# Performance work log

Measured on AMD Instinct MI355X. Metric: run time of the kernel, lower is better.

## Reference

```python
import jax, jax.numpy as jnp
import numpy as np

N_NODES = 100000
N_HEDGES = 25000
NNZ = 1600000
IN_CH = 128
HEADS_OUT = 128  # heads * out_channels = 8 * 16


def setup_inputs() -> dict:
    key = jax.random.key(0)
    k1, k2, k3, k4, k5, k6 = jax.random.split(key, 6)
    X = jax.random.normal(k1, (N_NODES, IN_CH), dtype=jnp.float32)
    Wlin = jax.random.normal(k2, (IN_CH, HEADS_OUT), dtype=jnp.float32) * (1.0 / np.sqrt(IN_CH))
    degE = jax.random.uniform(k3, (N_HEDGES, 1), dtype=jnp.float32)
    degV = jax.random.uniform(k4, (N_NODES, 1), dtype=jnp.float32)
    W = jnp.ones((N_HEDGES, 1), dtype=jnp.float32)
    g1_src = jax.random.randint(k5, (NNZ,), 0, N_NODES, dtype=jnp.int32)
    g1_dst = jax.random.randint(k6, (NNZ,), 0, N_HEDGES, dtype=jnp.int32)
    return {"X": X, "Wlin": Wlin, "degE": degE, "degV": degV, "W": W,
            "g1_src": g1_src, "g1_dst": g1_dst}


def reference(X, Wlin, degE, degV, W, g1_src, g1_dst):
    # Linear projection (no bias): [N, in_ch] @ [in_ch, heads*out] -> [N, HO]
    Xp = X @ Wlin
    # Stage 1: copy_u_sum over g1 (node -> hyperedge): out[e] = sum_{v in e} Xp[v]
    Xe = jax.ops.segment_sum(Xp[g1_src], g1_dst, num_segments=N_HEDGES)
    # Elementwise hyperedge scaling: degE then W (W is ones buffer in original)
    Xe = Xe * degE * W
    # Stage 2: copy_u_sum over g2 = g1^T (hyperedge -> node)
    Xv = jax.ops.segment_sum(Xe[g1_dst], g1_src, num_segments=N_NODES)
    # Node degree scaling
    Xv = Xv * degV
    return Xv
```

## Files before the change

kernel.cpp:

```cpp
#include <hip/hip_runtime.h>
#include <hip/hip_bf16.h>


#define CAPE 128
#define CAPV 64
#define LDK  136
#define RW   6250

typedef __attribute__((ext_vector_type(8))) short bf16x8;
typedef __attribute__((ext_vector_type(4))) float f32x4;
typedef __attribute__((ext_vector_type(8))) float f32x8;

__device__ __forceinline__ unsigned short f32_to_bf16(float f) {
    unsigned int u = __float_as_uint(f);
    u += 0x7FFFu + ((u >> 16) & 1u);
    return (unsigned short)(u >> 16);
}
__device__ __forceinline__ float bf16_to_f32(unsigned short h) {
    return __uint_as_float(((unsigned int)h) << 16);
}


__device__ __forceinline__ void scan_body(unsigned char* __restrict__ h8, int n,
                                          int b, int nch, int* __restrict__ cnt) {
    int run = 0;
    for (int c0 = 0; c0 < nch; c0 += 16) {
        unsigned char v[16];
#pragma unroll
        for (int j = 0; j < 16; ++j)
            v[j] = h8[(long)(c0 + j) * n + b];
        unsigned char w[16];
#pragma unroll
        for (int j = 0; j < 16; ++j) {
            w[j] = (unsigned char)run;
            run += v[j];
        }
#pragma unroll
        for (int j = 0; j < 16; ++j)
            h8[(long)(c0 + j) * n + b] = w[j];
    }
    cnt[b] = run;
}

__device__ __forceinline__ void hist_body(unsigned int* __restrict__ s32,
                                          const int* __restrict__ key, int nnz,
                                          unsigned int* __restrict__ hist,
                                          int n4, int ch, int c, int w0, int w1,
                                          int tid) {
    const int nw = w1 - w0;
    for (int i = tid; i < nw; i += 256) s32[i] = 0;
    __syncthreads();
    int e0 = c * ch, e1 = e0 + ch; if (e1 > nnz) e1 = nnz;
    for (int e = e0 + tid; e < e1; e += 256) {
        int k = key[e];
        int w = k >> 2;
        if (w >= w0 && w < w1)
            atomicAdd(&s32[w - w0], 1u << ((k & 3) * 8));
    }
    __syncthreads();
    for (int i = tid; i < nw; i += 256)
        hist[(long)c * n4 + w0 + i] = s32[i];
}

__device__ __forceinline__ void scatV_body(unsigned int* __restrict__ c32,
                                           const int* __restrict__ src,
                                           const int* __restrict__ dst, int nnz,
                                           const unsigned char* __restrict__ histV8,
                                           unsigned short* __restrict__ adjV,
                                           int nV4, int chv, int c, int r, int tid) {
    const int w0 = r * RW;
    int w1 = w0 + RW; if (w1 > nV4) w1 = nV4;
    const int nw = w1 - w0;
    const unsigned int* brow = (const unsigned int*)histV8 + (long)c * nV4 + w0;
    for (int i = tid; i < nw; i += 256) c32[i] = brow[i];
    __syncthreads();
    int e0 = c * chv, e1 = e0 + chv; if (e1 > nnz) e1 = nnz;
    for (int e = e0 + tid; e < e1; e += 256) {
        int k = src[e];
        int w = k >> 2;
        if (w < w0 || w >= w1) continue;
        int sh = (k & 3) * 8;
        unsigned int old = atomicAdd(&c32[w - w0], 1u << sh);
        int slot = (old >> sh) & 0xFF;
        if (slot < CAPV) adjV[(long)k * CAPV + slot] = (unsigned short)dst[e];
    }
}

__device__ __forceinline__ void gatherE_body(int id, int tid,
                                             const unsigned short* __restrict__ Xp,
                                             const int* __restrict__ cntE,
                                             const int* __restrict__ adjE,
                                             const float* __restrict__ degE,
                                             const float* __restrict__ Wbuf,
                                             unsigned short* __restrict__ Xe,
                                             int nE) {
    int t = id * 256 + tid;
    int e = t >> 4;
    if (e >= nE) return;
    int c = (t & 15) << 3;
    int len = cntE[e];
    if (len > CAPE) len = CAPE;
    const int* adj = adjE + (long)e * CAPE;
    float acc[8];
#pragma unroll
    for (int q = 0; q < 8; ++q) acc[q] = 0.f;

    int i = 0;
    for (; i + 16 <= len; i += 16) {
        int4 a0 = *(const int4*)(adj + i);
        int4 a1 = *(const int4*)(adj + i + 4);
        int4 a2 = *(const int4*)(adj + i + 8);
        int4 a3 = *(const int4*)(adj + i + 12);
        int v[16] = {a0.x, a0.y, a0.z, a0.w, a1.x, a1.y, a1.z, a1.w,
                     a2.x, a2.y, a2.z, a2.w, a3.x, a3.y, a3.z, a3.w};
        bf16x8 h[16];
#pragma unroll
        for (int j = 0; j < 16; ++j)
            h[j] = *(const bf16x8*)(Xp + (long)v[j] * 128 + c);
#pragma unroll
        for (int j = 0; j < 16; ++j)
#pragma unroll
            for (int q = 0; q < 8; ++q)
                acc[q] += bf16_to_f32((unsigned short)h[j][q]);
    }
    for (; i + 8 <= len; i += 8) {
        int4 a0 = *(const int4*)(adj + i);
        int4 a1 = *(const int4*)(adj + i + 4);
        int v[8] = {a0.x, a0.y, a0.z, a0.w, a1.x, a1.y, a1.z, a1.w};
        bf16x8 h[8];
#pragma unroll
        for (int j = 0; j < 8; ++j)
            h[j] = *(const bf16x8*)(Xp + (long)v[j] * 128 + c);
#pragma unroll
        for (int j = 0; j < 8; ++j)
#pragma unroll
            for (int q = 0; q < 8; ++q)
                acc[q] += bf16_to_f32((unsigned short)h[j][q]);
    }
    for (; i + 4 <= len; i += 4) {
        int4 a0 = *(const int4*)(adj + i);
        int v[4] = {a0.x, a0.y, a0.z, a0.w};
        bf16x8 h[4];
#pragma unroll
        for (int j = 0; j < 4; ++j)
            h[j] = *(const bf16x8*)(Xp + (long)v[j] * 128 + c);
#pragma unroll
        for (int j = 0; j < 4; ++j)
#pragma unroll
            for (int q = 0; q < 8; ++q)
                acc[q] += bf16_to_f32((unsigned short)h[j][q]);
    }
    for (; i < len; ++i) {
        int v = adj[i];
        bf16x8 h = *(const bf16x8*)(Xp + (long)v * 128 + c);
#pragma unroll
        for (int q = 0; q < 8; ++q)
            acc[q] += bf16_to_f32((unsigned short)h[q]);
    }

    float sc = degE[e] * Wbuf[e];
    bf16x8 o;
#pragma unroll
    for (int q = 0; q < 8; ++q) o[q] = (short)f32_to_bf16(acc[q] * sc);
    *(bf16x8*)(Xe + (long)e * 128 + c) = o;
}

__device__ __forceinline__ void gatherV_body(int id, int tid,
                                             const unsigned short* __restrict__ Xe,
                                             const int* __restrict__ cntV,
                                             const unsigned short* __restrict__ adjV,
                                             const float* __restrict__ degV,
                                             float* __restrict__ out,
                                             int vLo, int vHi) {
    int t = id * 256 + tid;
    int v = vLo + (t >> 4);
    if (v >= vHi) return;
    int c = (t & 15) << 3;
    int len = cntV[v];
    if (len > CAPV) len = CAPV;
    const unsigned short* adj = adjV + (long)v * CAPV;
    float acc[8];
#pragma unroll
    for (int q = 0; q < 8; ++q) acc[q] = 0.f;

    int i = 0;
    for (; i + 16 <= len; i += 16) {
        ushort4 a0 = *(const ushort4*)(adj + i);
        ushort4 a1 = *(const ushort4*)(adj + i + 4);
        ushort4 a2 = *(const ushort4*)(adj + i + 8);
        ushort4 a3 = *(const ushort4*)(adj + i + 12);
        int e[16] = {a0.x, a0.y, a0.z, a0.w, a1.x, a1.y, a1.z, a1.w,
                     a2.x, a2.y, a2.z, a2.w, a3.x, a3.y, a3.z, a3.w};
        bf16x8 h[16];
#pragma unroll
        for (int j = 0; j < 16; ++j)
            h[j] = *(const bf16x8*)(Xe + (long)e[j] * 128 + c);
#pragma unroll
        for (int j = 0; j < 16; ++j)
#pragma unroll
            for (int q = 0; q < 8; ++q)
                acc[q] += bf16_to_f32((unsigned short)h[j][q]);
    }
    for (; i + 8 <= len; i += 8) {
        ushort4 a0 = *(const ushort4*)(adj + i);
        ushort4 a1 = *(const ushort4*)(adj + i + 4);
        int e[8] = {a0.x, a0.y, a0.z, a0.w, a1.x, a1.y, a1.z, a1.w};
        bf16x8 h[8];
#pragma unroll
        for (int j = 0; j < 8; ++j)
            h[j] = *(const bf16x8*)(Xe + (long)e[j] * 128 + c);
#pragma unroll
        for (int j = 0; j < 8; ++j)
#pragma unroll
            for (int q = 0; q < 8; ++q)
                acc[q] += bf16_to_f32((unsigned short)h[j][q]);
    }
    for (; i + 4 <= len; i += 4) {
        ushort4 a0 = *(const ushort4*)(adj + i);
        int e[4] = {a0.x, a0.y, a0.z, a0.w};
        bf16x8 h[4];
#pragma unroll
        for (int j = 0; j < 4; ++j)
            h[j] = *(const bf16x8*)(Xe + (long)e[j] * 128 + c);
#pragma unroll
        for (int j = 0; j < 4; ++j)
#pragma unroll
            for (int q = 0; q < 8; ++q)
                acc[q] += bf16_to_f32((unsigned short)h[j][q]);
    }
    for (; i < len; ++i) {
        int e = adj[i];
        bf16x8 h = *(const bf16x8*)(Xe + (long)e * 128 + c);
#pragma unroll
        for (int q = 0; q < 8; ++q)
            acc[q] += bf16_to_f32((unsigned short)h[q]);
    }

    float sc = degV[v];
    f32x8 o;
#pragma unroll
    for (int q = 0; q < 8; ++q) o[q] = acc[q] * sc;
    *(f32x8*)(out + (long)v * 128 + c) = o;
}


__global__ __launch_bounds__(256) void k_init(const float* __restrict__ Wl,
                                              unsigned short* __restrict__ Wt) {
    int idx = blockIdx.x * 256 + threadIdx.x;
    if (idx < 128 * 128) {
        int n = idx >> 7, k = idx & 127;
        Wt[idx] = f32_to_bf16(Wl[k * 128 + n]);
    }
}

__global__ __launch_bounds__(256) void k_gemm_histE(
    const float* __restrict__ X, const unsigned short* __restrict__ Wt,
    unsigned short* __restrict__ Xp, int nrows, int nGemm,
    const int* __restrict__ keyE, int nnz,
    unsigned int* __restrict__ histE32, int nE4, int che, int nchE)
{
    __shared__ union {
        struct { unsigned short Xs[64 * LDK]; unsigned short Wt[128 * LDK]; } g;
        unsigned int s32[RW];
    } sm;

    int bid = blockIdx.x;
    const int tid = threadIdx.x;

    if (bid < nGemm) {
        const int row0 = bid * 64;
        for (int base = tid * 4; base < 64 * 128; base += 1024) {
            int r = base >> 7, c = base & 127;
            float4 v = make_float4(0.f, 0.f, 0.f, 0.f);
            if (row0 + r < nrows) v = *(const float4*)(X + (long)(row0 + r) * 128 + c);
            ushort4 h;
            h.x = f32_to_bf16(v.x); h.y = f32_to_bf16(v.y);
            h.z = f32_to_bf16(v.z); h.w = f32_to_bf16(v.w);
            *(ushort4*)(sm.g.Xs + r * LDK + c) = h;
        }
        for (int base = tid * 4; base < 128 * 128; base += 1024) {
            int n = base >> 7, k = base & 127;
            ushort4 h = *(const ushort4*)(Wt + base);
            *(ushort4*)(sm.g.Wt + n * LDK + k) = h;
        }
        __syncthreads();

        const int w    = tid >> 6;
        const int lane = tid & 63;
        const int m    = lane & 15;
        const int quad = lane >> 4;

        f32x4 acc[8];
#pragma unroll
        for (int ct = 0; ct < 8; ++ct) acc[ct] = (f32x4){0.f, 0.f, 0.f, 0.f};

#pragma unroll
        for (int kk = 0; kk < 4; ++kk) {
            bf16x8 a = *(const bf16x8*)(sm.g.Xs + (w * 16 + m) * LDK + kk * 32 + quad * 8);
#pragma unroll
            for (int ct = 0; ct < 8; ++ct) {
                bf16x8 b = *(const bf16x8*)(sm.g.Wt + (ct * 16 + m) * LDK + kk * 32 + quad * 8);
                acc[ct] = __builtin_amdgcn_mfma_f32_16x16x32_bf16(a, b, acc[ct], 0, 0, 0);
            }
        }
#pragma unroll
        for (int ct = 0; ct < 8; ++ct) {
#pragma unroll
            for (int r = 0; r < 4; ++r) {
                int row = row0 + w * 16 + quad * 4 + r;
                if (row < nrows)
                    Xp[(long)row * 128 + ct * 16 + m] = f32_to_bf16(acc[ct][r]);
            }
        }
        return;
    }

    int c = bid - nGemm;
    if (c < nchE)
        hist_body(sm.s32, keyE, nnz, histE32, nE4, che, c, 0, nE4, tid);
}

__global__ __launch_bounds__(256) void k_scanE_histV(
    unsigned char* __restrict__ histE8, int* __restrict__ cntE,
    int nE, int nchE, int nScanE,
    const int* __restrict__ keyV, int nnz,
    unsigned int* __restrict__ histV32, int nV4, int chv, int nchV)
{
    __shared__ unsigned int s32[RW];
    int bid = blockIdx.x;
    const int tid = threadIdx.x;
    if (bid < nScanE) {
        int t = bid * 256 + tid;
        if (t < nE) scan_body(histE8, nE, t, nchE, cntE);
        return;
    }
    bid -= nScanE;
    const int c = bid % nchV, r = bid / nchV;
    const int w0 = r * RW;
    int w1 = w0 + RW; if (w1 > nV4) w1 = nV4;
    hist_body(s32, keyV, nnz, histV32, nV4, chv, c, w0, w1, tid);
}

__global__ __launch_bounds__(256) void k_scatE_scanV(
    const int* __restrict__ src, const int* __restrict__ dst, int nnz,
    const unsigned char* __restrict__ histE8, int* __restrict__ adjE,
    int nE4, int che, int nchE,
    unsigned char* __restrict__ histV8, int* __restrict__ cntV, int nV, int nchV)
{
    __shared__ unsigned int c32[RW];
    int bid = blockIdx.x;
    const int tid = threadIdx.x;
    if (bid < nchE) {
        const int c = bid;
        const unsigned int* brow = (const unsigned int*)histE8 + (long)c * nE4;
        for (int i = tid; i < nE4; i += 256) c32[i] = brow[i];
        __syncthreads();
        int e0 = c * che, e1 = e0 + che; if (e1 > nnz) e1 = nnz;
        for (int e = e0 + tid; e < e1; e += 256) {
            int k = dst[e];
            int sh = (k & 3) * 8;
            unsigned int old = atomicAdd(&c32[k >> 2], 1u << sh);
            int slot = (old >> sh) & 0xFF;
            if (slot < CAPE) adjE[(long)k * CAPE + slot] = src[e];
        }
        return;
    }
    int t = (bid - nchE) * 256 + tid;
    if (t < nV) scan_body(histV8, nV, t, nchV, cntV);
}

__global__ __launch_bounds__(256) void k_gathE_scatV(
    const unsigned short* __restrict__ Xp, const int* __restrict__ cntE,
    const int* __restrict__ adjE, const float* __restrict__ degE,
    const float* __restrict__ Wbuf, unsigned short* __restrict__ Xe,
    int nE, int nGathE,
    const int* __restrict__ src, const int* __restrict__ dst, int nnz,
    const unsigned char* __restrict__ histV8, unsigned short* __restrict__ adjV,
    int nV4, int chv, int nchV)
{
    __shared__ unsigned int c32[RW];
    int bid = blockIdx.x;
    const int tid = threadIdx.x;
    if (bid < nGathE) {
        gatherE_body(bid, tid, Xp, cntE, adjE, degE, Wbuf, Xe, nE);
        return;
    }
    bid -= nGathE;
    const int c = bid % nchV, r = bid / nchV;
    scatV_body(c32, src, dst, nnz, histV8, adjV, nV4, chv, c, r, tid);
}

__global__ __launch_bounds__(256) void k_gatherV(const unsigned short* __restrict__ Xe,
                                                 const int* __restrict__ cntV,
                                                 const unsigned short* __restrict__ adjV,
                                                 const float* __restrict__ degV,
                                                 float* __restrict__ out,
                                                 int vLo, int vHi) {
    gatherV_body(blockIdx.x, threadIdx.x, Xe, cntV, adjV, degV, out, vLo, vHi);
}

__global__ __launch_bounds__(256) void zero_f4(float4* __restrict__ p, int n4) {
    int i = blockIdx.x * 256 + threadIdx.x;
    if (i < n4) p[i] = make_float4(0.f, 0.f, 0.f, 0.f);
}

__global__ __launch_bounds__(256) void gemm_xw_f32(const float* __restrict__ X,
                                                   const float* __restrict__ Wl,
                                                   float* __restrict__ Xp,
                                                   int nrows) {
    __shared__ float Xs[32 * 128];
    const int tid = threadIdx.x;
    const int row0 = blockIdx.x * 32;
    for (int i = tid * 4; i < 32 * 128; i += 256 * 4) {
        int r = row0 + (i >> 7);
        float4 v = make_float4(0.f, 0.f, 0.f, 0.f);
        if (r < nrows) v = *(const float4*)(X + (long)row0 * 128 + i);
        *(float4*)(Xs + i) = v;
    }
    __syncthreads();
    const int col = tid & 127;
    const int rg  = (tid >> 7) * 16;
    float acc[16];
#pragma unroll
    for (int r = 0; r < 16; ++r) acc[r] = 0.f;
    for (int k = 0; k < 128; k += 4) {
        const float w0 = Wl[(k + 0) * 128 + col];
        const float w1 = Wl[(k + 1) * 128 + col];
        const float w2 = Wl[(k + 2) * 128 + col];
        const float w3 = Wl[(k + 3) * 128 + col];
#pragma unroll
        for (int r = 0; r < 16; ++r) {
            float4 x = *(const float4*)(Xs + (rg + r) * 128 + k);
            acc[r] = fmaf(x.w, w3, fmaf(x.z, w2, fmaf(x.y, w1, fmaf(x.x, w0, acc[r]))));
        }
    }
#pragma unroll
    for (int r = 0; r < 16; ++r) {
        int row = row0 + rg + r;
        if (row < nrows) Xp[(long)row * 128 + col] = acc[r];
    }
}

__global__ __launch_bounds__(256) void scatter_to_hedges(const float* __restrict__ Xp,
                                                         const int* __restrict__ src,
                                                         const int* __restrict__ dst,
                                                         float* __restrict__ Xe,
                                                         int nnz) {
    int t = blockIdx.x * 256 + threadIdx.x;
    int e = t >> 5;
    if (e >= nnz) return;
    int c = (t & 31) << 2;
    int s = src[e], d = dst[e];
    float4 v = *(const float4*)(Xp + (long)s * 128 + c);
    float* o = Xe + (long)d * 128 + c;
    atomicAdd(o + 0, v.x); atomicAdd(o + 1, v.y);
    atomicAdd(o + 2, v.z); atomicAdd(o + 3, v.w);
}

__global__ __launch_bounds__(256) void scatter_to_nodes(const float* __restrict__ Xe,
                                                        const int* __restrict__ src,
                                                        const int* __restrict__ dst,
                                                        const float* __restrict__ degE,
                                                        const float* __restrict__ Wbuf,
                                                        const float* __restrict__ degV,
                                                        float* __restrict__ out,
                                                        int nnz) {
    int t = blockIdx.x * 256 + threadIdx.x;
    int e = t >> 5;
    if (e >= nnz) return;
    int c = (t & 31) << 2;
    int s = src[e], d = dst[e];
    float sc = degE[d] * Wbuf[d] * degV[s];
    float4 v = *(const float4*)(Xe + (long)d * 128 + c);
    float* o = out + (long)s * 128 + c;
    atomicAdd(o + 0, v.x * sc); atomicAdd(o + 1, v.y * sc);
    atomicAdd(o + 2, v.z * sc); atomicAdd(o + 3, v.w * sc);
}

extern "C" void kernel_launch(void* const* d_in, const int* in_sizes, int n_in,
                              void* d_out, int out_size, void* d_ws, size_t ws_size,
                              hipStream_t stream) {
    const float* X    = (const float*)d_in[0];
    const float* Wlin = (const float*)d_in[1];
    const float* degE = (const float*)d_in[2];
    const float* degV = (const float*)d_in[3];
    const float* Wbuf = (const float*)d_in[4];
    const int* g1_src = (const int*)d_in[5];
    const int* g1_dst = (const int*)d_in[6];

    const int nE  = in_sizes[2];
    const int nV  = in_sizes[3];
    const int nnz = in_sizes[5];

    float* out = (float*)d_out;
    char* ws = (char*)d_ws;

    auto layout_size = [&](int cE, int cV) -> size_t {
        size_t o = 0;
        o += (size_t)nE * CAPE * 4;
        o += (size_t)nV * CAPV * 2;
        o += (size_t)nE * 4 + (size_t)nV * 4;
        size_t he = (size_t)cE * nE;
        size_t xe = (size_t)nE * 128 * 2;
        o += (he > xe) ? he : xe;
        o += (size_t)cV * nV;
        o += 128 * 128 * 2;
        o += 4096;
        return o;
    };

    int nchE = 256, nchV = 256;
    if (layout_size(nchE, nchV) > ws_size) { nchE = 256; nchV = 128; }
    if (layout_size(nchE, nchV) > ws_size) { nchE = 128; nchV = 128; }
    if (layout_size(nchE, nchV) > ws_size) { nchE = 64;  nchV = 64;  }

    const int nE4 = nE >> 2, nV4 = nV >> 2;
    const bool eligible = ((nE & 3) == 0) && ((nV & 3) == 0) && (nE4 <= RW) &&
                          layout_size(nchE, nchV) <= ws_size;

    if (eligible) {
        size_t boff = 0;
        auto alloc = [&](size_t bytes) -> char* {
            char* p = ws + boff;
            boff += (bytes + 255) & ~(size_t)255;
            return p;
        };
        int* adjE            = (int*)alloc((size_t)nE * CAPE * 4);
        unsigned short* adjV = (unsigned short*)alloc((size_t)nV * CAPV * 2);
        int* cntE            = (int*)alloc((size_t)nE * 4);
        int* cntV            = (int*)alloc((size_t)nV * 4);
        size_t he = (size_t)nchE * nE;
        size_t xe = (size_t)nE * 128 * 2;
        char* region1         = alloc((he > xe) ? he : xe);
        unsigned char* histE8 = (unsigned char*)region1;
        unsigned short* Xe    = (unsigned short*)region1;
        unsigned char* histV8 = (unsigned char*)alloc((size_t)nchV * nV);
        unsigned short* Wt    = (unsigned short*)alloc((size_t)128 * 128 * 2);

        unsigned short* Xp_bf = (unsigned short*)d_out;

        const int nrV = (nV4 + RW - 1) / RW;
        const int che = (nnz + nchE - 1) / nchE;
        const int chv = (nnz + nchV - 1) / nchV;

        k_init<<<64, 256, 0, stream>>>(Wlin, Wt);

        int nGemm = (nV + 63) / 64;
        k_gemm_histE<<<nGemm + nchE, 256, 0, stream>>>(
            X, Wt, Xp_bf, nV, nGemm,
            g1_dst, nnz, (unsigned int*)histE8, nE4, che, nchE);

        int nScanE = (nE + 255) / 256;
        k_scanE_histV<<<nScanE + nchV * nrV, 256, 0, stream>>>(
            histE8, cntE, nE, nchE, nScanE,
            g1_src, nnz, (unsigned int*)histV8, nV4, chv, nchV);

        int nScanV = (nV + 255) / 256;
        k_scatE_scanV<<<nchE + nScanV, 256, 0, stream>>>(
            g1_src, g1_dst, nnz, histE8, adjE, nE4, che, nchE,
            histV8, cntV, nV, nchV);

        int nGathE = (nE * 16 + 255) / 256;
        k_gathE_scatV<<<nGathE + nchV * nrV, 256, 0, stream>>>(
            Xp_bf, cntE, adjE, degE, Wbuf, Xe, nE, nGathE,
            g1_src, g1_dst, nnz, histV8, adjV, nV4, chv, nchV);

        int nGathV = (nV * 16 + 255) / 256;
        k_gatherV<<<nGathV, 256, 0, stream>>>(Xe, cntV, adjV, degV, out, 0, nV);
    } else {
        float* XeF = (float*)d_ws;
        float* Xp  = out;
        int n4 = nE * 128 / 4;
        zero_f4<<<(n4 + 255) / 256, 256, 0, stream>>>((float4*)XeF, n4);
        gemm_xw_f32<<<(nV + 31) / 32, 256, 0, stream>>>(X, Wlin, Xp, nV);
        long th = (long)nnz * 32;
        scatter_to_hedges<<<(int)((th + 255) / 256), 256, 0, stream>>>(Xp, g1_src, g1_dst,
                                                                       XeF, nnz);
        int m4 = out_size / 4;
        zero_f4<<<(m4 + 255) / 256, 256, 0, stream>>>((float4*)out, m4);
        scatter_to_nodes<<<(int)((th + 255) / 256), 256, 0, stream>>>(XeF, g1_src, g1_dst,
                                                                      degE, Wbuf, degV,
                                                                      out, nnz);
    }
}
```

Before: 326.2 us.

## Store projected features in column-sliced layout and gather hyperedges per slice

After: 394.7 us. +21.0%, slower.

```diff
diff --git a/kernel.cpp b/kernel.cpp
--- a/kernel.cpp
+++ b/kernel.cpp
@@ -10,6 +10,8 @@
 typedef __attribute__((ext_vector_type(8))) short bf16x8;
 typedef __attribute__((ext_vector_type(4))) float f32x4;
 typedef __attribute__((ext_vector_type(8))) float f32x8;
+typedef __attribute__((ext_vector_type(4))) int i32x4;
+typedef __attribute__((ext_vector_type(4))) unsigned short u16x4;
 
 __device__ __forceinline__ unsigned short f32_to_bf16(float f) {
     unsigned int u = __float_as_uint(f);
@@ -82,22 +84,25 @@
         int sh = (k & 3) * 8;
         unsigned int old = atomicAdd(&c32[w - w0], 1u << sh);
         int slot = (old >> sh) & 0xFF;
-        if (slot < CAPV) adjV[(long)k * CAPV + slot] = (unsigned short)dst[e];
-    }
-}
-
-__device__ __forceinline__ void gatherE_body(int id, int tid,
-                                             const unsigned short* __restrict__ Xp,
-                                             const int* __restrict__ cntE,
-                                             const int* __restrict__ adjE,
-                                             const float* __restrict__ degE,
-                                             const float* __restrict__ Wbuf,
-                                             unsigned short* __restrict__ Xe,
-                                             int nE) {
-    int t = id * 256 + tid;
-    int e = t >> 4;
+        if (slot < CAPV)
+            __builtin_nontemporal_store((unsigned short)dst[e],
+                                        adjV + (long)k * CAPV + slot);
+    }
+}
+
+__device__ __forceinline__ void gatherE_sliced(int bid, int tid,
+                                               const unsigned short* __restrict__ Xp,
+                                               const int* __restrict__ cntE,
+                                               const int* __restrict__ adjE,
+                                               const float* __restrict__ degE,
+                                               const float* __restrict__ Wbuf,
+                                               unsigned short* __restrict__ Xe,
+                                               int nE, long sstride) {
+    const int slice = bid & 7;
+    int e = ((bid >> 3) << 7) + (tid >> 1);
     if (e >= nE) return;
-    int c = (t & 15) << 3;
+    const int c = (tid & 1) << 3;
+    const unsigned short* Xs = Xp + (long)slice * sstride;
     int len = cntE[e];
     if (len > CAPE) len = CAPE;
     const int* adj = adjE + (long)e * CAPE;
@@ -107,16 +112,16 @@
 
     int i = 0;
     for (; i + 16 <= len; i += 16) {
-        int4 a0 = *(const int4*)(adj + i);
-        int4 a1 = *(const int4*)(adj + i + 4);
-        int4 a2 = *(const int4*)(adj + i + 8);
-        int4 a3 = *(const int4*)(adj + i + 12);
+        i32x4 a0 = __builtin_nontemporal_load((const i32x4*)(adj + i));
+        i32x4 a1 = __builtin_nontemporal_load((const i32x4*)(adj + i + 4));
+        i32x4 a2 = __builtin_nontemporal_load((const i32x4*)(adj + i + 8));
+        i32x4 a3 = __builtin_nontemporal_load((const i32x4*)(adj + i + 12));
         int v[16] = {a0.x, a0.y, a0.z, a0.w, a1.x, a1.y, a1.z, a1.w,
                      a2.x, a2.y, a2.z, a2.w, a3.x, a3.y, a3.z, a3.w};
         bf16x8 h[16];
 #pragma unroll
         for (int j = 0; j < 16; ++j)
-            h[j] = *(const bf16x8*)(Xp + (long)v[j] * 128 + c);
+            h[j] = *(const bf16x8*)(Xs + (long)v[j] * 16 + c);
 #pragma unroll
         for (int j = 0; j < 16; ++j)
 #pragma unroll
@@ -124,13 +129,13 @@
                 acc[q] += bf16_to_f32((unsigned short)h[j][q]);
     }
     for (; i + 8 <= len; i += 8) {
-        int4 a0 = *(const int4*)(adj + i);
-        int4 a1 = *(const int4*)(adj + i + 4);
+        i32x4 a0 = __builtin_nontemporal_load((const i32x4*)(adj + i));
+        i32x4 a1 = __builtin_nontemporal_load((const i32x4*)(adj + i + 4));
         int v[8] = {a0.x, a0.y, a0.z, a0.w, a1.x, a1.y, a1.z, a1.w};
         bf16x8 h[8];
 #pragma unroll
         for (int j = 0; j < 8; ++j)
-            h[j] = *(const bf16x8*)(Xp + (long)v[j] * 128 + c);
+            h[j] = *(const bf16x8*)(Xs + (long)v[j] * 16 + c);
 #pragma unroll
         for (int j = 0; j < 8; ++j)
 #pragma unroll
@@ -138,12 +143,12 @@
                 acc[q] += bf16_to_f32((unsigned short)h[j][q]);
     }
     for (; i + 4 <= len; i += 4) {
-        int4 a0 = *(const int4*)(adj + i);
+        i32x4 a0 = __builtin_nontemporal_load((const i32x4*)(adj + i));
         int v[4] = {a0.x, a0.y, a0.z, a0.w};
         bf16x8 h[4];
 #pragma unroll
         for (int j = 0; j < 4; ++j)
-            h[j] = *(const bf16x8*)(Xp + (long)v[j] * 128 + c);
+            h[j] = *(const bf16x8*)(Xs + (long)v[j] * 16 + c);
 #pragma unroll
         for (int j = 0; j < 4; ++j)
 #pragma unroll
@@ -152,7 +157,7 @@
     }
     for (; i < len; ++i) {
         int v = adj[i];
-        bf16x8 h = *(const bf16x8*)(Xp + (long)v * 128 + c);
+        bf16x8 h = *(const bf16x8*)(Xs + (long)v * 16 + c);
 #pragma unroll
         for (int q = 0; q < 8; ++q)
             acc[q] += bf16_to_f32((unsigned short)h[q]);
@@ -162,7 +167,7 @@
     bf16x8 o;
 #pragma unroll
     for (int q = 0; q < 8; ++q) o[q] = (short)f32_to_bf16(acc[q] * sc);
-    *(bf16x8*)(Xe + (long)e * 128 + c) = o;
+    __builtin_nontemporal_store(o, (bf16x8*)(Xe + (long)e * 128 + slice * 16 + c));
 }
 
 __device__ __forceinline__ void gatherV_body(int id, int tid,
@@ -185,10 +190,10 @@
 
     int i = 0;
     for (; i + 16 <= len; i += 16) {
-        ushort4 a0 = *(const ushort4*)(adj + i);
-        ushort4 a1 = *(const ushort4*)(adj + i + 4);
-        ushort4 a2 = *(const ushort4*)(adj + i + 8);
-        ushort4 a3 = *(const ushort4*)(adj + i + 12);
+        u16x4 a0 = *(const u16x4*)(adj + i);
+        u16x4 a1 = *(const u16x4*)(adj + i + 4);
+        u16x4 a2 = *(const u16x4*)(adj + i + 8);
+        u16x4 a3 = *(const u16x4*)(adj + i + 12);
         int e[16] = {a0.x, a0.y, a0.z, a0.w, a1.x, a1.y, a1.z, a1.w,
                      a2.x, a2.y, a2.z, a2.w, a3.x, a3.y, a3.z, a3.w};
         bf16x8 h[16];
@@ -202,8 +207,8 @@
                 acc[q] += bf16_to_f32((unsigned short)h[j][q]);
     }
     for (; i + 8 <= len; i += 8) {
-        ushort4 a0 = *(const ushort4*)(adj + i);
-        ushort4 a1 = *(const ushort4*)(adj + i + 4);
+        u16x4 a0 = *(const u16x4*)(adj + i);
+        u16x4 a1 = *(const u16x4*)(adj + i + 4);
         int e[8] = {a0.x, a0.y, a0.z, a0.w, a1.x, a1.y, a1.z, a1.w};
         bf16x8 h[8];
 #pragma unroll
@@ -216,7 +221,7 @@
                 acc[q] += bf16_to_f32((unsigned short)h[j][q]);
     }
     for (; i + 4 <= len; i += 4) {
-        ushort4 a0 = *(const ushort4*)(adj + i);
+        u16x4 a0 = *(const u16x4*)(adj + i);
         int e[4] = {a0.x, a0.y, a0.z, a0.w};
         bf16x8 h[4];
 #pragma unroll
@@ -240,7 +245,7 @@
     f32x8 o;
 #pragma unroll
     for (int q = 0; q < 8; ++q) o[q] = acc[q] * sc;
-    *(f32x8*)(out + (long)v * 128 + c) = o;
+    __builtin_nontemporal_store(o, (f32x8*)(out + (long)v * 128 + c));
 }
 
 
@@ -309,7 +314,8 @@
             for (int r = 0; r < 4; ++r) {
                 int row = row0 + w * 16 + quad * 4 + r;
                 if (row < nrows)
-                    Xp[(long)row * 128 + ct * 16 + m] = f32_to_bf16(acc[ct][r]);
+                    Xp[(long)ct * nrows * 16 + (long)row * 16 + m] =
+                        f32_to_bf16(acc[ct][r]);
             }
         }
         return;
@@ -373,7 +379,7 @@
     const unsigned short* __restrict__ Xp, const int* __restrict__ cntE,
     const int* __restrict__ adjE, const float* __restrict__ degE,
     const float* __restrict__ Wbuf, unsigned short* __restrict__ Xe,
-    int nE, int nGathE,
+    int nE, int nGathE, long sstride,
     const int* __restrict__ src, const int* __restrict__ dst, int nnz,
     const unsigned char* __restrict__ histV8, unsigned short* __restrict__ adjV,
     int nV4, int chv, int nchV)
@@ -382,7 +388,7 @@
     int bid = blockIdx.x;
     const int tid = threadIdx.x;
     if (bid < nGathE) {
-        gatherE_body(bid, tid, Xp, cntE, adjE, degE, Wbuf, Xe, nE);
+        gatherE_sliced(bid, tid, Xp, cntE, adjE, degE, Wbuf, Xe, nE, sstride);
         return;
     }
     bid -= nGathE;
@@ -542,6 +548,7 @@
         const int nrV = (nV4 + RW - 1) / RW;
         const int che = (nnz + nchE - 1) / nchE;
         const int chv = (nnz + nchV - 1) / nchV;
+        const long sstride = (long)nV * 16;
 
         k_init<<<64, 256, 0, stream>>>(Wlin, Wt);
 
@@ -560,9 +567,9 @@
             g1_src, g1_dst, nnz, histE8, adjE, nE4, che, nchE,
             histV8, cntV, nV, nchV);
 
-        int nGathE = (nE * 16 + 255) / 256;
+        int nGathE = 8 * ((nE + 127) / 128);
         k_gathE_scatV<<<nGathE + nchV * nrV, 256, 0, stream>>>(
-            Xp_bf, cntE, adjE, degE, Wbuf, Xe, nE, nGathE,
+            Xp_bf, cntE, adjE, degE, Wbuf, Xe, nE, nGathE, sstride,
             g1_src, g1_dst, nnz, histV8, adjV, nV4, chv, nchV);
 
         int nGathV = (nV * 16 + 255) / 256;
```

## Split gathers into column halves and overlap second-half hedge gather with node gather

Applied to the files above, without the earlier changes.

New measurement: 327.2 us. About the same (+0.3%).

```diff
diff --git a/kernel.cpp b/kernel.cpp
--- a/kernel.cpp
+++ b/kernel.cpp
@@ -86,7 +86,7 @@
     }
 }
 
-__device__ __forceinline__ void gatherE_body(int id, int tid,
+__device__ __forceinline__ void gatherE_half(int id, int tid, int colBase,
                                              const unsigned short* __restrict__ Xp,
                                              const int* __restrict__ cntE,
                                              const int* __restrict__ adjE,
@@ -95,9 +95,9 @@
                                              unsigned short* __restrict__ Xe,
                                              int nE) {
     int t = id * 256 + tid;
-    int e = t >> 4;
+    int e = t >> 3;
     if (e >= nE) return;
-    int c = (t & 15) << 3;
+    int c = ((t & 7) << 3) + colBase;
     int len = cntE[e];
     if (len > CAPE) len = CAPE;
     const int* adj = adjE + (long)e * CAPE;
@@ -165,17 +165,17 @@
     *(bf16x8*)(Xe + (long)e * 128 + c) = o;
 }
 
-__device__ __forceinline__ void gatherV_body(int id, int tid,
+__device__ __forceinline__ void gatherV_half(int id, int tid, int colBase,
                                              const unsigned short* __restrict__ Xe,
                                              const int* __restrict__ cntV,
                                              const unsigned short* __restrict__ adjV,
                                              const float* __restrict__ degV,
                                              float* __restrict__ out,
-                                             int vLo, int vHi) {
+                                             int nV) {
     int t = id * 256 + tid;
-    int v = vLo + (t >> 4);
-    if (v >= vHi) return;
-    int c = (t & 15) << 3;
+    int v = t >> 3;
+    if (v >= nV) return;
+    int c = ((t & 7) << 3) + colBase;
     int len = cntV[v];
     if (len > CAPV) len = CAPV;
     const unsigned short* adj = adjV + (long)v * CAPV;
@@ -382,12 +382,38 @@
     int bid = blockIdx.x;
     const int tid = threadIdx.x;
     if (bid < nGathE) {
-        gatherE_body(bid, tid, Xp, cntE, adjE, degE, Wbuf, Xe, nE);
+        gatherE_half(bid, tid, 0, Xp, cntE, adjE, degE, Wbuf, Xe, nE);
         return;
     }
     bid -= nGathE;
     const int c = bid % nchV, r = bid / nchV;
     scatV_body(c32, src, dst, nnz, histV8, adjV, nV4, chv, c, r, tid);
+}
+
+__global__ __launch_bounds__(256) void k_gathE_gathV(
+    const unsigned short* __restrict__ Xp, const int* __restrict__ cntE,
+    const int* __restrict__ adjE, const float* __restrict__ degE,
+    const float* __restrict__ Wbuf, unsigned short* __restrict__ Xe,
+    int nE, int nGathE,
+    const int* __restrict__ cntV, const unsigned short* __restrict__ adjV,
+    const float* __restrict__ degV, float* __restrict__ out, int nV)
+{
+    int bid = blockIdx.x;
+    const int tid = threadIdx.x;
+    if (bid < nGathE) {
+        gatherE_half(bid, tid, 64, Xp, cntE, adjE, degE, Wbuf, Xe, nE);
+        return;
+    }
+    gatherV_half(bid - nGathE, tid, 0, Xe, cntV, adjV, degV, out, nV);
+}
+
+__global__ __launch_bounds__(256) void k_gathE_only(
+    const unsigned short* __restrict__ Xp, const int* __restrict__ cntE,
+    const int* __restrict__ adjE, const float* __restrict__ degE,
+    const float* __restrict__ Wbuf, unsigned short* __restrict__ Xe,
+    int nE, int colBase)
+{
+    gatherE_half(blockIdx.x, threadIdx.x, colBase, Xp, cntE, adjE, degE, Wbuf, Xe, nE);
 }
 
 __global__ __launch_bounds__(256) void k_gatherV(const unsigned short* __restrict__ Xe,
@@ -395,8 +421,8 @@
                                                  const unsigned short* __restrict__ adjV,
                                                  const float* __restrict__ degV,
                                                  float* __restrict__ out,
-                                                 int vLo, int vHi) {
-    gatherV_body(blockIdx.x, threadIdx.x, Xe, cntV, adjV, degV, out, vLo, vHi);
+                                                 int nV, int colBase) {
+    gatherV_half(blockIdx.x, threadIdx.x, colBase, Xe, cntV, adjV, degV, out, nV);
 }
 
 __global__ __launch_bounds__(256) void zero_f4(float4* __restrict__ p, int n4) {
@@ -495,7 +521,7 @@
     float* out = (float*)d_out;
     char* ws = (char*)d_ws;
 
-    auto layout_size = [&](int cE, int cV) -> size_t {
+    auto layout_size = [&](int cE, int cV, bool xpWs) -> size_t {
         size_t o = 0;
         o += (size_t)nE * CAPE * 4;
         o += (size_t)nV * CAPV * 2;
@@ -505,18 +531,27 @@
         o += (he > xe) ? he : xe;
         o += (size_t)cV * nV;
         o += 128 * 128 * 2;
-        o += 4096;
+        if (xpWs) o += (size_t)nV * 128 * 2;
+        o += 8192;
         return o;
     };
 
+    bool xpWs = true;
     int nchE = 256, nchV = 256;
-    if (layout_size(nchE, nchV) > ws_size) { nchE = 256; nchV = 128; }
-    if (layout_size(nchE, nchV) > ws_size) { nchE = 128; nchV = 128; }
-    if (layout_size(nchE, nchV) > ws_size) { nchE = 64;  nchV = 64;  }
+    auto fits = [&](int a, int b, bool x) { return layout_size(a, b, x) <= ws_size; };
+    if (!fits(nchE, nchV, xpWs)) { nchE = 256; nchV = 128; }
+    if (!fits(nchE, nchV, xpWs)) { nchE = 128; nchV = 128; }
+    if (!fits(nchE, nchV, xpWs)) { nchE = 64;  nchV = 64;  }
+    if (!fits(nchE, nchV, xpWs)) {
+        xpWs = false; nchE = 256; nchV = 256;
+        if (!fits(nchE, nchV, xpWs)) { nchE = 256; nchV = 128; }
+        if (!fits(nchE, nchV, xpWs)) { nchE = 128; nchV = 128; }
+        if (!fits(nchE, nchV, xpWs)) { nchE = 64;  nchV = 64;  }
+    }
 
     const int nE4 = nE >> 2, nV4 = nV >> 2;
     const bool eligible = ((nE & 3) == 0) && ((nV & 3) == 0) && (nE4 <= RW) &&
-                          layout_size(nchE, nchV) <= ws_size;
+                          fits(nchE, nchV, xpWs);
 
     if (eligible) {
         size_t boff = 0;
@@ -536,8 +571,9 @@
         unsigned short* Xe    = (unsigned short*)region1;
         unsigned char* histV8 = (unsigned char*)alloc((size_t)nchV * nV);
         unsigned short* Wt    = (unsigned short*)alloc((size_t)128 * 128 * 2);
-
-        unsigned short* Xp_bf = (unsigned short*)d_out;
+        unsigned short* Xp_bf = xpWs
+            ? (unsigned short*)alloc((size_t)nV * 128 * 2)
+            : (unsigned short*)d_out;
 
         const int nrV = (nV4 + RW - 1) / RW;
         const int che = (nnz + nchE - 1) / nchE;
@@ -560,13 +596,23 @@
             g1_src, g1_dst, nnz, histE8, adjE, nE4, che, nchE,
             histV8, cntV, nV, nchV);
 
-        int nGathE = (nE * 16 + 255) / 256;
-        k_gathE_scatV<<<nGathE + nchV * nrV, 256, 0, stream>>>(
-            Xp_bf, cntE, adjE, degE, Wbuf, Xe, nE, nGathE,
+        int nGE = (nE * 8 + 255) / 256;
+        int nGV = (nV * 8 + 255) / 256;
+        k_gathE_scatV<<<nGE + nchV * nrV, 256, 0, stream>>>(
+            Xp_bf, cntE, adjE, degE, Wbuf, Xe, nE, nGE,
             g1_src, g1_dst, nnz, histV8, adjV, nV4, chv, nchV);
 
-        int nGathV = (nV * 16 + 255) / 256;
-        k_gatherV<<<nGathV, 256, 0, stream>>>(Xe, cntV, adjV, degV, out, 0, nV);
+        if (xpWs) {
+            k_gathE_gathV<<<nGE + nGV, 256, 0, stream>>>(
+                Xp_bf, cntE, adjE, degE, Wbuf, Xe, nE, nGE,
+                cntV, adjV, degV, out, nV);
+            k_gatherV<<<nGV, 256, 0, stream>>>(Xe, cntV, adjV, degV, out, nV, 64);
+        } else {
+            k_gathE_only<<<nGE, 256, 0, stream>>>(Xp_bf, cntE, adjE, degE, Wbuf,
+                                                  Xe, nE, 64);
+            k_gatherV<<<nGV, 256, 0, stream>>>(Xe, cntV, adjV, degV, out, nV, 0);
+            k_gatherV<<<nGV, 256, 0, stream>>>(Xe, cntV, adjV, degV, out, nV, 64);
+        }
     } else {
         float* XeF = (float*)d_ws;
         float* Xp  = out;
```
